# Kernel optimization log

Measured on AMD Instinct MI355X. Metric: run time of the kernel, lower is better.

## Reference

```python
import jax, jax.numpy as jnp
import numpy as np

EPS = 1e-3  # Keras LayerNormalization default epsilon


def _gru_seq(x_tbf, W, U, b):
    """Keras GRU (reset_after=True). x_tbf: [T,B,F], W: [F,3U], U: [U,3U], b: [2,3U]."""
    bi, br = b[0], b[1]
    xw = jnp.einsum('tbf,fg->tbg', x_tbf, W) + bi  # precompute input projections
    B = x_tbf.shape[1]
    units = U.shape[0]
    h0 = jnp.zeros((B, units), x_tbf.dtype)

    def step(h, xw_t):
        inner = h @ U + br
        xz, xr, xh = jnp.split(xw_t, 3, axis=-1)
        rz, rr, rh = jnp.split(inner, 3, axis=-1)
        z = jax.nn.sigmoid(xz + rz)
        r = jax.nn.sigmoid(xr + rr)
        hh = jnp.tanh(xh + r * rh)
        h_new = z * h + (1.0 - z) * hh
        return h_new, h_new

    _, hs = jax.lax.scan(step, h0, xw)
    return hs  # [T,B,U]


def setup_inputs() -> dict:
    key = jax.random.key(0)
    B, T, F, Uu = 64, 1024, 256, 512
    ks = jax.random.split(key, 8)
    s = 0.05
    return {
        'x': jax.random.normal(ks[0], (B, T, F), jnp.float32),
        'Wf': jax.random.normal(ks[1], (F, 3 * Uu), jnp.float32) * s,
        'Uf': jax.random.normal(ks[2], (Uu, 3 * Uu), jnp.float32) * s,
        'bf': jnp.zeros((2, 3 * Uu), jnp.float32),
        'Wb': jax.random.normal(ks[3], (F, 3 * Uu), jnp.float32) * s,
        'Ub': jax.random.normal(ks[4], (Uu, 3 * Uu), jnp.float32) * s,
        'bb': jnp.zeros((2, 3 * Uu), jnp.float32),
        'Wp': jax.random.normal(ks[5], (F, 2 * Uu), jnp.float32) * s,
        'gamma': jnp.ones((2 * Uu,), jnp.float32),
        'beta': jnp.zeros((2 * Uu,), jnp.float32),
    }


def reference(x, Wf, Uf, bf, Wb, Ub, bb, Wp, gamma, beta):
    x_t = jnp.transpose(x, (1, 0, 2))  # [T,B,F]
    hf = _gru_seq(x_t, Wf, Uf, bf)
    hb = _gru_seq(x_t[::-1], Wb, Ub, bb)[::-1]
    gru_out = jnp.transpose(jnp.concatenate([hf, hb], axis=-1), (1, 0, 2))  # [B,T,2U]
    residual = x @ Wp  # projection (F != 2U)
    y = gru_out + residual
    mu = jnp.mean(y, axis=-1, keepdims=True)
    var = jnp.var(y, axis=-1, keepdims=True)
    return gamma * (y - mu) * jax.lax.rsqrt(var + EPS) + beta
```

## Files before the change

kernel.cpp:

```cpp
#include <hip/hip_runtime.h>
#include <stdint.h>
#include <stddef.h>

#define TB 1024
#define NBATCH 64
#define FD 256
#define UD 512
#define G3 1536
#define OD 1024

#define WS_BAR 0
#define WS_H 512
#define WS_RESID (512 + 4 * NBATCH * UD * 2)

#define NREC 64
#define NRESID 16384

typedef __bf16 v8bf __attribute__((ext_vector_type(8)));
typedef float v4f __attribute__((ext_vector_type(4)));

__device__ __forceinline__ v4f mfma16(v8bf a, v8bf b, v4f c) {
  return __builtin_amdgcn_mfma_f32_16x16x32_bf16(a, b, c, 0, 0, 0);
}

__device__ __forceinline__ float sigf(float x) {
  return 1.0f / (1.0f + __expf(-x));
}
__device__ __forceinline__ float tanhf_fast(float x) {
  float ax = fabsf(x);
  float e = __expf(-2.0f * ax);
  float t = (1.0f - e) / (1.0f + e);
  return copysignf(t, x);
}

__device__ __forceinline__ v8bf cvt8(const float* p) {
  float4 a = *(const float4*)p;
  float4 b = *(const float4*)(p + 4);
  v8bf r;
  r[0] = (__bf16)a.x; r[1] = (__bf16)a.y; r[2] = (__bf16)a.z; r[3] = (__bf16)a.w;
  r[4] = (__bf16)b.x; r[5] = (__bf16)b.y; r[6] = (__bf16)b.z; r[7] = (__bf16)b.w;
  return r;
}

struct XW { v4f a0, a1, a2; };

__device__ __forceinline__ XW compute_xw(const float* __restrict__ x,
                                         const v8bf wfr[8][3],
                                         float bi0, float bi1, float bi2,
                                         int b, int t, int quad) {
  XW r;
  r.a0 = v4f{bi0, bi0, bi0, bi0};
  r.a1 = v4f{bi1, bi1, bi1, bi1};
  r.a2 = v4f{bi2, bi2, bi2, bi2};
  const float* xp = x + ((size_t)b * TB + t) * FD + quad * 8;
#pragma unroll
  for (int ki = 0; ki < 8; ++ki) {
    v8bf xa = cvt8(xp + ki * 32);
    r.a0 = mfma16(xa, wfr[ki][0], r.a0);
    r.a1 = mfma16(xa, wfr[ki][1], r.a1);
    r.a2 = mfma16(xa, wfr[ki][2], r.a2);
  }
  return r;
}

__device__ void recurrent_body(const float* __restrict__ x,
                               const float* __restrict__ Wd,
                               const float* __restrict__ Ud,
                               const float* __restrict__ bd,
                               float* __restrict__ out,
                               char* __restrict__ ws, int bx) {
  const int dir = bx >> 5;
  const int blk = bx & 31;
  const int j0 = blk * 16;
  const int tid = threadIdx.x;
  const int lane = tid & 63;
  const int col16 = lane & 15;
  const int quad = lane >> 4;
  const int m0 = (tid >> 6) * 16;

  uint32_t* flags = (uint32_t*)(ws + WS_BAR) + dir * 32;
  __bf16* h0 = (__bf16*)(ws + WS_H) + (size_t)dir * 2 * NBATCH * UD;
  __bf16* h1 = h0 + NBATCH * UD;

  v8bf ufr[16][3];
#pragma unroll
  for (int ki = 0; ki < 16; ++ki) {
#pragma unroll
    for (int g = 0; g < 3; ++g) {
      const float* p = Ud + (size_t)(ki * 32 + quad * 8) * G3 + g * UD + j0 + col16;
      v8bf v;
#pragma unroll
      for (int e = 0; e < 8; ++e) v[e] = (__bf16)p[(size_t)e * G3];
      ufr[ki][g] = v;
    }
  }
  v8bf wfr[8][3];
#pragma unroll
  for (int ki = 0; ki < 8; ++ki) {
#pragma unroll
    for (int g = 0; g < 3; ++g) {
      const float* p = Wd + (size_t)(ki * 32 + quad * 8) * G3 + g * UD + j0 + col16;
      v8bf v;
#pragma unroll
      for (int e = 0; e < 8; ++e) v[e] = (__bf16)p[(size_t)e * G3];
      wfr[ki][g] = v;
    }
  }
  const float bi0 = bd[0 * UD + j0 + col16];
  const float bi1 = bd[1 * UD + j0 + col16];
  const float bi2 = bd[2 * UD + j0 + col16];
  const float br0 = bd[G3 + 0 * UD + j0 + col16];
  const float br1 = bd[G3 + 1 * UD + j0 + col16];
  const float br2 = bd[G3 + 2 * UD + j0 + col16];

  const int tstep = dir ? -1 : 1;
  int t = dir ? (TB - 1) : 0;
  XW cur = compute_xw(x, wfr, bi0, bi1, bi2, m0 + col16, t, quad);

  float hold[4] = {0.f, 0.f, 0.f, 0.f};

  int p = 0;
  for (int s = 0; s < TB; ++s) {
    const __bf16* hcur = (p == 0) ? h0 : h1;
    __bf16* hnxt = (p == 0) ? h1 : h0;

    v4f au0 = v4f{br0, br0, br0, br0};
    v4f au1 = v4f{br1, br1, br1, br1};
    v4f au2 = v4f{br2, br2, br2, br2};
    if (s > 0) {
      const __bf16* hrow = hcur + (size_t)(m0 + col16) * UD + quad * 8;
#pragma unroll
      for (int ki = 0; ki < 16; ++ki) {
        v8bf ha = *(const v8bf*)(hrow + ki * 32);
        au0 = mfma16(ha, ufr[ki][0], au0);
        au1 = mfma16(ha, ufr[ki][1], au1);
        au2 = mfma16(ha, ufr[ki][2], au2);
      }
    }

    float hn[4];
#pragma unroll
    for (int r = 0; r < 4; ++r) {
      float z = sigf(cur.a0[r] + au0[r]);
      float rg = sigf(cur.a1[r] + au1[r]);
      float hh = tanhf_fast(cur.a2[r] + rg * au2[r]);
      float v = z * hold[r] + (1.0f - z) * hh;
      hn[r] = v;
      hold[r] = v;
    }
    const int tcur = t;

    if (s < TB - 1) {
#pragma unroll
      for (int r = 0; r < 4; ++r) {
        hnxt[(size_t)(m0 + quad * 4 + r) * UD + j0 + col16] = (__bf16)hn[r];
      }
      __syncthreads();
      if (tid == 0) {
        __hip_atomic_store(&flags[blk], (uint32_t)(s + 1), __ATOMIC_RELEASE,
                           __HIP_MEMORY_SCOPE_AGENT);
      }
#pragma unroll
      for (int r = 0; r < 4; ++r) {
        const int brow = m0 + quad * 4 + r;
        __builtin_nontemporal_store(
            hn[r], out + ((size_t)brow * TB + tcur) * OD + dir * UD + j0 + col16);
      }
      t += tstep;
      XW nxt = compute_xw(x, wfr, bi0, bi1, bi2, m0 + col16, t, quad);

      const uint32_t target = (uint32_t)(s + 1);
      for (;;) {
        uint32_t f = __hip_atomic_load(&flags[lane & 31], __ATOMIC_RELAXED,
                                       __HIP_MEMORY_SCOPE_AGENT);
        if (__ballot(f >= target) == ~0ull) break;
        __builtin_amdgcn_s_sleep(1);
      }
      __builtin_amdgcn_fence(__ATOMIC_ACQUIRE, "agent");

      cur = nxt;
      p ^= 1;
    } else {
#pragma unroll
      for (int r = 0; r < 4; ++r) {
        const int brow = m0 + quad * 4 + r;
        __builtin_nontemporal_store(
            hn[r], out + ((size_t)brow * TB + tcur) * OD + dir * UD + j0 + col16);
      }
    }
  }
}

__device__ void resid_body(const float* __restrict__ x,
                           const float* __restrict__ Wp,
                           __bf16* __restrict__ resid, int rb) {
  const int mb = rb & 1023;
  const int nb = rb >> 10;
  const int tid = threadIdx.x;
  const int lane = tid & 63;
  const int col16 = lane & 15;
  const int quad = lane >> 4;
  const int wave = tid >> 6;
  const int wm = wave & 1;
  const int wn = wave >> 1;
  const int rowbase = mb * 64 + wm * 32;
  const int colbase = nb * 64 + wn * 32;

  v4f acc[2][2];
#pragma unroll
  for (int i = 0; i < 2; ++i)
#pragma unroll
    for (int j = 0; j < 2; ++j) acc[i][j] = v4f{0.f, 0.f, 0.f, 0.f};

#pragma unroll
  for (int ki = 0; ki < 8; ++ki) {
    v8bf a0 = cvt8(x + (size_t)(rowbase + col16) * FD + ki * 32 + quad * 8);
    v8bf a1 = cvt8(x + (size_t)(rowbase + 16 + col16) * FD + ki * 32 + quad * 8);
    v8bf b0, b1;
#pragma unroll
    for (int e = 0; e < 8; ++e) {
      const float* wp = Wp + (size_t)(ki * 32 + quad * 8 + e) * OD + colbase + col16;
      b0[e] = (__bf16)wp[0];
      b1[e] = (__bf16)wp[16];
    }
    acc[0][0] = mfma16(a0, b0, acc[0][0]);
    acc[0][1] = mfma16(a0, b1, acc[0][1]);
    acc[1][0] = mfma16(a1, b0, acc[1][0]);
    acc[1][1] = mfma16(a1, b1, acc[1][1]);
  }
#pragma unroll
  for (int mt = 0; mt < 2; ++mt)
#pragma unroll
    for (int nt = 0; nt < 2; ++nt)
#pragma unroll
      for (int r = 0; r < 4; ++r) {
        __builtin_nontemporal_store(
            (__bf16)acc[mt][nt][r],
            resid + (size_t)(rowbase + mt * 16 + quad * 4 + r) * OD + colbase +
                nt * 16 + col16);
      }
}

__global__ __launch_bounds__(256, 1) void mega_kernel(
    const float* __restrict__ x, const float* __restrict__ Wf,
    const float* __restrict__ Uf, const float* __restrict__ bf_,
    const float* __restrict__ Wb, const float* __restrict__ Ub,
    const float* __restrict__ bb_, const float* __restrict__ Wp,
    float* __restrict__ out, char* __restrict__ ws) {
  const int bx = blockIdx.x;
  if (bx < NREC) {
    const int dir = bx >> 5;
    recurrent_body(x, dir ? Wb : Wf, dir ? Ub : Uf, dir ? bb_ : bf_, out, ws, bx);
  } else {
    resid_body(x, Wp, (__bf16*)(ws + WS_RESID), bx - NREC);
  }
}

__global__ __launch_bounds__(256) void ln_kernel(
    const __bf16* __restrict__ resid, const float* __restrict__ gamma,
    const float* __restrict__ beta, float* __restrict__ out) {
  const int row = blockIdx.x * 4 + (threadIdx.x >> 6);
  const int lane = threadIdx.x & 63;
  const float* orow = out + (size_t)row * OD;
  const __bf16* rrow = resid + (size_t)row * OD;

  float y[16];
  float s = 0.f, s2 = 0.f;
#pragma unroll
  for (int i = 0; i < 16; ++i) {
    const int c = lane + 64 * i;
    float v = orow[c] + (float)rrow[c];
    y[i] = v;
    s += v;
    s2 += v * v;
  }
#pragma unroll
  for (int m = 32; m >= 1; m >>= 1) {
    s += __shfl_xor(s, m);
    s2 += __shfl_xor(s2, m);
  }
  const float mu = s * (1.0f / OD);
  const float var = s2 * (1.0f / OD) - mu * mu;
  const float rstd = rsqrtf(var + 1e-3f);
  float* wrow = out + (size_t)row * OD;
#pragma unroll
  for (int i = 0; i < 16; ++i) {
    const int c = lane + 64 * i;
    __builtin_nontemporal_store(gamma[c] * (y[i] - mu) * rstd + beta[c], wrow + c);
  }
}

extern "C" void kernel_launch(void* const* d_in, const int* in_sizes, int n_in,
                              void* d_out, int out_size, void* d_ws,
                              size_t ws_size, hipStream_t stream) {
  const float* x = (const float*)d_in[0];
  const float* Wf = (const float*)d_in[1];
  const float* Uf = (const float*)d_in[2];
  const float* bf_ = (const float*)d_in[3];
  const float* Wb = (const float*)d_in[4];
  const float* Ub = (const float*)d_in[5];
  const float* bb_ = (const float*)d_in[6];
  const float* Wp = (const float*)d_in[7];
  const float* gamma = (const float*)d_in[8];
  const float* beta = (const float*)d_in[9];
  float* out = (float*)d_out;
  char* ws = (char*)d_ws;

  hipMemsetAsync(ws, 0, 512, stream);

  mega_kernel<<<dim3(NREC + NRESID), dim3(256), 0, stream>>>(
      x, Wf, Uf, bf_, Wb, Ub, bb_, Wp, out, ws);

  ln_kernel<<<dim3(65536 / 4), dim3(256), 0, stream>>>(
      (const __bf16*)(ws + WS_RESID), gamma, beta, out);
}
```

Baseline: 10.27 ms.

## Replace block barrier with per-wave flags and atomic h exchange in GRU recurrence

Each wave now publishes its own slice of the hidden state with relaxed agent-scope atomic stores and signals its own flag, so the block-wide __syncthreads, release store, acquire fence and sleep in the spin loop are all dropped. Hidden-state reads switch to relaxed atomic 64-bit loads so they bypass stale cache lines without a fence. Each wave now waits only on the matching wave-row flags from the other 32 blocks. The point is to shorten the per-timestep critical path of the serial recurrence. The risk is memory ordering: it relies on s_waitcnt and relaxed atomics rather than formal release/acquire semantics.

```diff
diff --git a/kernel.cpp b/kernel.cpp
--- a/kernel.cpp
+++ b/kernel.cpp
@@ -10,8 +10,8 @@
 #define OD 1024
 
 #define WS_BAR 0
-#define WS_H 512
-#define WS_RESID (512 + 4 * NBATCH * UD * 2)
+#define WS_H 4096
+#define WS_RESID (4096 + 4 * NBATCH * UD * 2)
 
 #define NREC 64
 #define NRESID 16384
@@ -76,9 +76,10 @@
   const int lane = tid & 63;
   const int col16 = lane & 15;
   const int quad = lane >> 4;
-  const int m0 = (tid >> 6) * 16;
-
-  uint32_t* flags = (uint32_t*)(ws + WS_BAR) + dir * 32;
+  const int wave = tid >> 6;
+  const int m0 = wave * 16;
+
+  uint32_t* flagsW = (uint32_t*)(ws + WS_BAR) + (dir * 4 + wave) * 32;
   __bf16* h0 = (__bf16*)(ws + WS_H) + (size_t)dir * 2 * NBATCH * UD;
   __bf16* h1 = h0 + NBATCH * UD;
 
@@ -131,10 +132,18 @@
       const __bf16* hrow = hcur + (size_t)(m0 + col16) * UD + quad * 8;
 #pragma unroll
       for (int ki = 0; ki < 16; ++ki) {
-        v8bf ha = *(const v8bf*)(hrow + ki * 32);
-        au0 = mfma16(ha, ufr[ki][0], au0);
-        au1 = mfma16(ha, ufr[ki][1], au1);
-        au2 = mfma16(ha, ufr[ki][2], au2);
+        const unsigned long long* hp =
+            (const unsigned long long*)(hrow + (size_t)ki * 32);
+        unsigned long long d0 = __hip_atomic_load(hp, __ATOMIC_RELAXED,
+                                                  __HIP_MEMORY_SCOPE_AGENT);
+        unsigned long long d1 = __hip_atomic_load(hp + 1, __ATOMIC_RELAXED,
+                                                  __HIP_MEMORY_SCOPE_AGENT);
+        union { unsigned long long q[2]; v8bf v; } u;
+        u.q[0] = d0;
+        u.q[1] = d1;
+        au0 = mfma16(u.v, ufr[ki][0], au0);
+        au1 = mfma16(u.v, ufr[ki][1], au1);
+        au2 = mfma16(u.v, ufr[ki][2], au2);
       }
     }
 
@@ -153,11 +162,15 @@
     if (s < TB - 1) {
 #pragma unroll
       for (int r = 0; r < 4; ++r) {
-        hnxt[(size_t)(m0 + quad * 4 + r) * UD + j0 + col16] = (__bf16)hn[r];
-      }
-      __syncthreads();
-      if (tid == 0) {
-        __hip_atomic_store(&flags[blk], (uint32_t)(s + 1), __ATOMIC_RELEASE,
+        __bf16 hb = (__bf16)hn[r];
+        unsigned short bits = __builtin_bit_cast(unsigned short, hb);
+        __hip_atomic_store(
+            (unsigned short*)&hnxt[(size_t)(m0 + quad * 4 + r) * UD + j0 + col16],
+            bits, __ATOMIC_RELAXED, __HIP_MEMORY_SCOPE_AGENT);
+      }
+      asm volatile("s_waitcnt vmcnt(0)" ::: "memory");
+      if (lane == 0) {
+        __hip_atomic_store(&flagsW[blk], (uint32_t)(s + 1), __ATOMIC_RELAXED,
                            __HIP_MEMORY_SCOPE_AGENT);
       }
 #pragma unroll
@@ -171,12 +184,10 @@
 
       const uint32_t target = (uint32_t)(s + 1);
       for (;;) {
-        uint32_t f = __hip_atomic_load(&flags[lane & 31], __ATOMIC_RELAXED,
+        uint32_t f = __hip_atomic_load(&flagsW[lane & 31], __ATOMIC_RELAXED,
                                        __HIP_MEMORY_SCOPE_AGENT);
         if (__ballot(f >= target) == ~0ull) break;
-        __builtin_amdgcn_s_sleep(1);
-      }
-      __builtin_amdgcn_fence(__ATOMIC_ACQUIRE, "agent");
+      }
 
       cur = nxt;
       p ^= 1;
@@ -306,7 +317,7 @@
   float* out = (float*)d_out;
   char* ws = (char*)d_ws;
 
-  hipMemsetAsync(ws, 0, 512, stream);
+  hipMemsetAsync(ws, 0, 2048, stream);
 
   mega_kernel<<<dim3(NREC + NRESID), dim3(256), 0, stream>>>(
       x, Wf, Uf, bf_, Wb, Ub, bb_, Wp, out, ws);
```

New measurement: 10.42 ms. No clear change (+1.4%).
